# Kernel tuning notes

Measured on AMD Instinct MI355X. Metric: run time of the kernel, lower is better.

The kernel has to match this reference:

```python
import jax, jax.numpy as jnp
import numpy as np

DECAY = 0.999
EPS = 1e-05
COMMITMENT_COST = 0.25
M, D = 1024, 256
B, H, W = 32, 32, 32


def setup_inputs() -> dict:
    key = jax.random.key(0)
    k1, k2 = jax.random.split(key)
    init_bound = 1.0 / M
    x = jax.random.normal(k1, (B, H, W, D), dtype=jnp.float32)
    embedding = jax.random.uniform(k2, (M, D), dtype=jnp.float32,
                                   minval=-init_bound, maxval=init_bound)
    ema_count = jnp.zeros((M,), dtype=jnp.float32)
    ema_weight = embedding  # buffer initialized as embedding.clone()
    return {"x": x, "embedding": embedding, "ema_count": ema_count,
            "ema_weight": ema_weight}


def reference(x, embedding, ema_count, ema_weight):
    Mn, Dn = embedding.shape
    x_flat = jax.lax.stop_gradient(x).reshape(-1, Dn)          # [N, D]
    N = x_flat.shape[0]

    # (-cdist)^2 == squared euclidean distance; argmin is the same.
    x_sq = jnp.sum(x_flat * x_flat, axis=-1, keepdims=True)    # [N, 1]
    e_sq = jnp.sum(embedding * embedding, axis=-1)             # [M]
    distances = x_sq - 2.0 * (x_flat @ embedding.T) + e_sq[None, :]  # [N, M]
    indices = jnp.argmin(distances, axis=-1)                   # [N]

    quantized = embedding[indices].reshape(x.shape)            # gather

    # one-hot column sums == scatter-add of ones; encodings.T @ x_flat == scatter-add rows
    counts = jnp.zeros((Mn,), x.dtype).at[indices].add(1.0)    # [M]
    dw = jnp.zeros((Mn, Dn), x.dtype).at[indices].add(x_flat)  # [M, D]

    new_count = DECAY * ema_count + (1.0 - DECAY) * counts
    n = jnp.sum(new_count)
    new_count = (new_count + EPS) / (n + Mn * EPS) * n
    new_weight = DECAY * ema_weight + (1.0 - DECAY) * dw
    new_embedding = new_weight / new_count[:, None]

    codebook_loss = jnp.mean((jax.lax.stop_gradient(x) - quantized) ** 2)
    e_latent_loss = jnp.mean((x - jax.lax.stop_gradient(quantized)) ** 2)
    commitment_loss = COMMITMENT_COST * e_latent_loss

    quantized_st = x + jax.lax.stop_gradient(quantized - x)    # straight-through

    avg_probs = counts / N
    perplexity = jnp.exp(-jnp.sum(avg_probs * jnp.log(avg_probs + 1e-10)))

    return (quantized_st, commitment_loss, codebook_loss, perplexity,
            new_embedding, new_count, new_weight)
```

## Files before the change

kernel.cpp:

```cpp
#include <hip/hip_runtime.h>
#include <cfloat>
#include <math.h>

#define N_TOK 32768
#define DIM   256
#define MCODE 1024

typedef unsigned short u16;
typedef unsigned long long u64;
typedef __attribute__((ext_vector_type(8))) short short8;
typedef __attribute__((ext_vector_type(4))) float f32x4;

constexpr float DECAY_ = 0.999f;
constexpr float OMD_   = (float)(1.0 - 0.999);
constexpr float EPS_   = 1e-5f;
constexpr float MEPS_  = (float)(1024 * 1e-5);

constexpr int WS_EH   = 0;
constexpr int WS_EL   = 131072;
constexpr int WS_ESQ  = 262144;
constexpr int WS_CNTI = 263168;
constexpr int WS_BI   = 264192;
constexpr int WS_LP   = 296960;
constexpr int WS_KEY  = 299008;

constexpr int OUT_Q        = 0;
constexpr int OUT_COMMIT   = 8388608;
constexpr int OUT_CODEBOOK = 8388609;
constexpr int OUT_PERP     = 8388610;
constexpr int OUT_NE       = 8388611;
constexpr int OUT_NC       = 8650755;
constexpr int OUT_NW       = 8651779;

static __device__ __forceinline__ u16 f2bf(float f) {
    unsigned u = __float_as_uint(f);
    unsigned r = (u + 0x7fff + ((u >> 16) & 1)) >> 16;
    return (u16)r;
}
static __device__ __forceinline__ float bf2f(u16 h) {
    return __uint_as_float(((unsigned)h) << 16);
}
static __device__ __forceinline__ void gl2lds16(const u16* g, char* l) {
    __builtin_amdgcn_global_load_lds(
        (const __attribute__((address_space(1))) unsigned int*)g,
        (__attribute__((address_space(3))) unsigned int*)l, 16, 0, 0);
}
static __device__ __forceinline__ unsigned fmap(float f) {
    unsigned u = __float_as_uint(f);
    return (u & 0x80000000u) ? ~u : (u | 0x80000000u);
}

static __device__ __forceinline__ void load_row8(const float* __restrict__ src,
                                                 int wave_id, int lane,
                                                 float* vv, size_t* o) {
    int rb = wave_id >> 6, kc = (wave_id >> 3) & 7, t = wave_id & 7;
    int row = rb * 128 + t * 16 + (lane & 15);
    int k   = kc * 32 + (lane >> 4) * 8;
    const float* s = &src[row * DIM + k];
    float4 v0 = *(const float4*)s, v1 = *(const float4*)(s + 4);
    vv[0]=v0.x; vv[1]=v0.y; vv[2]=v0.z; vv[3]=v0.w;
    vv[4]=v1.x; vv[5]=v1.y; vv[6]=v1.z; vv[7]=v1.w;
    *o = (size_t)wave_id * 512 + lane * 8;
}
static __device__ __forceinline__ void pack_wave_hi(const float* __restrict__ src,
                                                    u16* __restrict__ dh,
                                                    int wave_id, int lane) {
    float vv[8]; size_t o;
    load_row8(src, wave_id, lane, vv, &o);
    short8 hv;
#pragma unroll
    for (int j = 0; j < 8; ++j) hv[j] = (short)f2bf(vv[j]);
    *(short8*)&dh[o] = hv;
}
static __device__ __forceinline__ void pack_wave_hl(const float* __restrict__ src,
                                                    u16* __restrict__ dh,
                                                    u16* __restrict__ dl,
                                                    int wave_id, int lane) {
    float vv[8]; size_t o;
    load_row8(src, wave_id, lane, vv, &o);
    short8 hv, lv;
#pragma unroll
    for (int j = 0; j < 8; ++j) {
        u16 h = f2bf(vv[j]);
        hv[j] = (short)h;
        lv[j] = (short)f2bf(vv[j] - bf2f(h));
    }
    *(short8*)&dh[o] = hv;
    *(short8*)&dl[o] = lv;
}

__global__ __launch_bounds__(256) void vq_setup(const float* __restrict__ x,
                                                const float* __restrict__ emb,
                                                u16* __restrict__ xh,
                                                u16* __restrict__ eh,
                                                u16* __restrict__ el,
                                                float* __restrict__ esq,
                                                u64* __restrict__ keys,
                                                int* __restrict__ cnti) {
    const int b = blockIdx.x, tid = threadIdx.x;
    const int lane = tid & 63, w = tid >> 6;
    if (b < 4096) { pack_wave_hi(x, xh, b * 4 + w, lane); return; }
    const int p = b - 4096;
    if (p < 128) {
        pack_wave_hl(emb, eh, el, p * 4 + w, lane);
    } else if (p < 384) {
        int c = (p - 128) * 4 + w;
        float4 v = *(const float4*)&emb[c * DIM + lane * 4];
        float s = v.x * v.x + v.y * v.y + v.z * v.z + v.w * v.w;
#pragma unroll
        for (int off = 32; off; off >>= 1) s += __shfl_xor(s, off, 64);
        if (lane == 0) esq[c] = s;
    } else if (p < 512) {
        keys[(p - 384) * 256 + tid] = ~0ULL;
    } else {
#pragma unroll
        for (int i = 0; i < 4; ++i) cnti[i * 256 + tid] = 0;
    }
}

__global__ __launch_bounds__(256) void vq_scores_mfma(const u16* __restrict__ xh,
                                                      const u16* __restrict__ eh,
                                                      const u16* __restrict__ el,
                                                      const float* __restrict__ esq,
                                                      u64* __restrict__ keys) {
    __shared__ __align__(16) char smem[33792];
    const int tid  = threadIdx.x;
    const int lane = tid & 63, w = tid >> 6;
    const int wm = w & 1, wn = w >> 1;
    const int raw = blockIdx.x;
    const int rb = (raw >> 6) * 8 + (raw & 7);
    const int cs = (raw >> 3) & 7;

    const u16* gb0 = xh + (size_t)rb * 32768;
    const u16* gb1 = eh + (size_t)cs * 32768;
    const u16* gb2 = el + (size_t)cs * 32768;

    const short8* Ah = (const short8*)(smem);
    const short8* Bh = (const short8*)(smem + 8192);
    const short8* Bl = (const short8*)(smem + 16384);

    f32x4 acc[4][4];
#pragma unroll
    for (int i = 0; i < 4; ++i)
#pragma unroll
        for (int j = 0; j < 4; ++j) acc[i][j] = (f32x4)0.f;

    for (int kc = 0; kc < 8; ++kc) {
        __syncthreads();
#pragma unroll
        for (int j = 0; j < 6; ++j) {
            int t = w * 6 + j;
            int arr = t >> 3, slot = t & 7;
            const u16* g = (arr == 0 ? gb0 : (arr == 1 ? gb1 : gb2))
                           + kc * 4096 + slot * 512 + lane * 8;
            gl2lds16(g, smem + arr * 8192 + slot * 1024);
        }
        __syncthreads();

        short8 ah[4];
#pragma unroll
        for (int tm = 0; tm < 4; ++tm)
            ah[tm] = Ah[(wm * 4 + tm) * 64 + lane];
#pragma unroll
        for (int tn = 0; tn < 4; ++tn) {
            int bidx = (wn * 4 + tn) * 64 + lane;
            short8 bh = Bh[bidx], bl = Bl[bidx];
#pragma unroll
            for (int tm = 0; tm < 4; ++tm) {
                acc[tm][tn] = __builtin_amdgcn_mfma_f32_16x16x32_bf16(ah[tm], bh, acc[tm][tn], 0, 0, 0);
                acc[tm][tn] = __builtin_amdgcn_mfma_f32_16x16x32_bf16(ah[tm], bl, acc[tm][tn], 0, 0, 0);
            }
        }
    }

    __syncthreads();
    float* cv = (float*)smem;
    int*   ci = (int*)(smem + 16896);
    const int ln = lane & 15, quad = lane >> 4;
#pragma unroll
    for (int tm = 0; tm < 4; ++tm) {
        float bv[4];
        int   bi[4];
#pragma unroll
        for (int r = 0; r < 4; ++r) { bv[r] = FLT_MAX; bi[r] = 0; }
#pragma unroll
        for (int tn = 0; tn < 4; ++tn) {
            int c = cs * 128 + wn * 64 + tn * 16 + ln;
            float ec = esq[c];
#pragma unroll
            for (int r = 0; r < 4; ++r) {
                float d = fmaf(-2.f, acc[tm][tn][r], ec);
                if (d < bv[r]) { bv[r] = d; bi[r] = c; }
            }
        }
        int row0 = wm * 64 + tm * 16 + quad * 4;
        int slot = wn * 16 + ln;
#pragma unroll
        for (int r = 0; r < 4; ++r) {
            cv[(row0 + r) * 33 + slot] = bv[r];
            ci[(row0 + r) * 33 + slot] = bi[r];
        }
    }
    __syncthreads();
    if (tid < 128) {
        float bv = cv[tid * 33];
        int   bi = ci[tid * 33];
#pragma unroll
        for (int s = 1; s < 32; ++s) {
            float v = cv[tid * 33 + s];
            int  ix = ci[tid * 33 + s];
            if (v < bv || (v == bv && ix < bi)) { bv = v; bi = ix; }
        }
        u64 key = ((u64)fmap(bv) << 32) | (unsigned)bi;
        atomicMin(&keys[rb * 128 + tid], key);
    }
}

__global__ __launch_bounds__(256) void vq_quant(const float* __restrict__ x,
                                                const float* __restrict__ emb,
                                                const u64* __restrict__ keys,
                                                float* __restrict__ outq,
                                                int* __restrict__ cnti,
                                                int* __restrict__ bi_arr,
                                                float* __restrict__ lpart) {
    const int tid = threadIdx.x, lane = tid & 63, w = tid >> 6;
    const float4* x4 = (const float4*)x;
    const float4* e4 = (const float4*)emb;
    float4* o4 = (float4*)outq;
    float lacc = 0.f;
#pragma unroll
    for (int it = 0; it < 4; ++it) {
        int row = blockIdx.x * 16 + it * 4 + w;
        int bi = (int)(unsigned)(keys[row] & 0xffffffffULL);
        if (lane == 0) { atomicAdd(&cnti[bi], 1); bi_arr[row] = bi; }
        float4 xv = x4[row * 64 + lane];
        float4 ev = e4[bi * 64 + lane];
        float4 q;
        q.x = xv.x + (ev.x - xv.x);  q.y = xv.y + (ev.y - xv.y);
        q.z = xv.z + (ev.z - xv.z);  q.w = xv.w + (ev.w - xv.w);
        o4[row * 64 + lane] = q;
        float dx = xv.x - ev.x, dy = xv.y - ev.y, dz = xv.z - ev.z, dwv = xv.w - ev.w;
        lacc += dx * dx + dy * dy + dz * dz + dwv * dwv;
    }
#pragma unroll
    for (int off = 32; off; off >>= 1) lacc += __shfl_xor(lacc, off, 64);
    __shared__ float red[4];
    if (lane == 0) red[w] = lacc;
    __syncthreads();
    if (tid == 0) lpart[blockIdx.x] = red[0] + red[1] + red[2] + red[3];
}

#define MEGA_CAP 6144
__global__ __launch_bounds__(256) void vq_mega(const float* __restrict__ x,
                                               const float* __restrict__ ema_count,
                                               const float* __restrict__ ema_weight,
                                               const int* __restrict__ cnti,
                                               const int* __restrict__ bi_arr,
                                               const float* __restrict__ lpart,
                                               float* __restrict__ out) {
    const int m = blockIdx.x, tid = threadIdx.x;
    __shared__ float fs[256];
    __shared__ int list[MEGA_CAP];
    __shared__ int lcount;

    float rsum = 0.f;
#pragma unroll
    for (int i = 0; i < 4; ++i) rsum += ema_count[tid * 4 + i];
    fs[tid] = rsum;
    if (tid == 0) lcount = 0;
    __syncthreads();
    for (int s = 128; s; s >>= 1) { if (tid < s) fs[tid] += fs[tid + s]; __syncthreads(); }
    const float n = DECAY_ * fs[0] + OMD_ * (float)N_TOK;
    __syncthreads();

    const int4* b4 = (const int4*)bi_arr;
#pragma unroll 4
    for (int i = tid; i < N_TOK / 4; i += 256) {
        int4 v = b4[i];
        if (v.x == m) { int p = atomicAdd(&lcount, 1); if (p < MEGA_CAP) list[p] = 4 * i; }
        if (v.y == m) { int p = atomicAdd(&lcount, 1); if (p < MEGA_CAP) list[p] = 4 * i + 1; }
        if (v.z == m) { int p = atomicAdd(&lcount, 1); if (p < MEGA_CAP) list[p] = 4 * i + 2; }
        if (v.w == m) { int p = atomicAdd(&lcount, 1); if (p < MEGA_CAP) list[p] = 4 * i + 3; }
    }
    __syncthreads();
    const int nm = lcount;
    float dwsum;
    if (nm <= MEGA_CAP) {
        float a0 = 0.f, a1 = 0.f, a2 = 0.f, a3 = 0.f;
        int i = 0;
        for (; i + 4 <= nm; i += 4) {
            a0 += x[list[i]     * DIM + tid];
            a1 += x[list[i + 1] * DIM + tid];
            a2 += x[list[i + 2] * DIM + tid];
            a3 += x[list[i + 3] * DIM + tid];
        }
        for (; i < nm; ++i) a0 += x[list[i] * DIM + tid];
        dwsum = (a0 + a1) + (a2 + a3);
    } else {
        __shared__ int chunk[256];
        float a0 = 0.f;
        for (int base = 0; base < N_TOK; base += 256) {
            __syncthreads();
            chunk[tid] = bi_arr[base + tid];
            __syncthreads();
            for (int j = 0; j < 256; ++j)
                if (chunk[j] == m) a0 += x[(base + j) * DIM + tid];
        }
        dwsum = a0;
    }

    float raw_m = DECAY_ * ema_count[m] + OMD_ * (float)nm;
    float ncm = (raw_m + EPS_) / (n + MEPS_) * n;
    float nw = DECAY_ * ema_weight[m * DIM + tid] + OMD_ * dwsum;
    out[OUT_NW + m * DIM + tid] = nw;
    out[OUT_NE + m * DIM + tid] = nw / ncm;
    if (tid == 0) out[OUT_NC + m] = ncm;

    if (m == 0) {
        float ent = 0.f;
#pragma unroll
        for (int i = 0; i < 4; ++i) {
            float p = (float)cnti[tid * 4 + i] / (float)N_TOK;
            ent += p * logf(p + 1e-10f);
        }
        __syncthreads();
        fs[tid] = ent;
        __syncthreads();
        for (int s = 128; s; s >>= 1) { if (tid < s) fs[tid] += fs[tid + s]; __syncthreads(); }
        float entr = fs[0];
        __syncthreads();
        float ls = 0.f;
#pragma unroll
        for (int k = 0; k < 8; ++k) ls += lpart[tid + 256 * k];
        fs[tid] = ls;
        __syncthreads();
        for (int s = 128; s; s >>= 1) { if (tid < s) fs[tid] += fs[tid + s]; __syncthreads(); }
        if (tid == 0) {
            float mean = fs[0] / (float)(N_TOK * DIM);
            out[OUT_COMMIT]   = 0.25f * mean;
            out[OUT_CODEBOOK] = mean;
            out[OUT_PERP]     = expf(-entr);
        }
    }
}

extern "C" void kernel_launch(void* const* d_in, const int* in_sizes, int n_in,
                              void* d_out, int out_size, void* d_ws, size_t ws_size,
                              hipStream_t stream) {
    const float* x          = (const float*)d_in[0];
    const float* emb        = (const float*)d_in[1];
    const float* ema_count  = (const float*)d_in[2];
    const float* ema_weight = (const float*)d_in[3];
    float* out = (float*)d_out;
    float* wf  = (float*)d_ws;

    u16* xh = (u16*)d_out;
    u16* eh = (u16*)(wf + WS_EH);
    u16* el = (u16*)(wf + WS_EL);

    float* esq    = wf + WS_ESQ;
    int*   cnti   = (int*)(wf + WS_CNTI);
    int*   bi_arr = (int*)(wf + WS_BI);
    float* lpart  = wf + WS_LP;
    u64*   keys   = (u64*)(wf + WS_KEY);

    vq_setup<<<4609, 256, 0, stream>>>(x, emb, xh, eh, el, esq, keys, cnti);
    vq_scores_mfma<<<2048, 256, 0, stream>>>(xh, eh, el, esq, keys);
    vq_quant<<<2048, 256, 0, stream>>>(x, emb, keys, out, cnti, bi_arr, lpart);
    vq_mega<<<MCODE, 256, 0, stream>>>(x, ema_count, ema_weight, cnti, bi_arr,
                                       lpart, out);
}
```

Before: 162.3 us.

## Double-buffer LDS staging in MFMA score kernel to overlap loads with compute

The score GEMM kernel now keeps two LDS buffers and prefetches the chunk two K-steps ahead with async global-to-LDS loads. Manual vmcnt waits and raw barriers replace the per-iteration pair of __syncthreads, and all fragments are read into registers before the barrier so the next stage can be issued into the same buffer. MFMA issue gets raised wave priority. This is meant to hide global load latency behind the MFMAs, at the cost of 48KB of LDS per block (lower occupancy) and fragile hand-written wait counts.

```diff
diff --git a/kernel.cpp b/kernel.cpp
--- a/kernel.cpp
+++ b/kernel.cpp
@@ -123,7 +123,7 @@
                                                       const u16* __restrict__ el,
                                                       const float* __restrict__ esq,
                                                       u64* __restrict__ keys) {
-    __shared__ __align__(16) char smem[33792];
+    __shared__ __align__(16) char smem[49152];
     const int tid  = threadIdx.x;
     const int lane = tid & 63, w = tid >> 6;
     const int wm = w & 1, wn = w >> 1;
@@ -135,43 +135,65 @@
     const u16* gb1 = eh + (size_t)cs * 32768;
     const u16* gb2 = el + (size_t)cs * 32768;
 
-    const short8* Ah = (const short8*)(smem);
-    const short8* Bh = (const short8*)(smem + 8192);
-    const short8* Bl = (const short8*)(smem + 16384);
-
-    f32x4 acc[4][4];
-#pragma unroll
-    for (int i = 0; i < 4; ++i)
-#pragma unroll
-        for (int j = 0; j < 4; ++j) acc[i][j] = (f32x4)0.f;
-
-    for (int kc = 0; kc < 8; ++kc) {
-        __syncthreads();
+    auto STAGE = [&](int KC, int BUF) {
 #pragma unroll
         for (int j = 0; j < 6; ++j) {
             int t = w * 6 + j;
             int arr = t >> 3, slot = t & 7;
             const u16* g = (arr == 0 ? gb0 : (arr == 1 ? gb1 : gb2))
-                           + kc * 4096 + slot * 512 + lane * 8;
-            gl2lds16(g, smem + arr * 8192 + slot * 1024);
-        }
-        __syncthreads();
-
-        short8 ah[4];
+                           + KC * 4096 + slot * 512 + lane * 8;
+            gl2lds16(g, smem + BUF * 24576 + arr * 8192 + slot * 1024);
+        }
+    };
+
+    f32x4 acc[4][4];
+#pragma unroll
+    for (int i = 0; i < 4; ++i)
+#pragma unroll
+        for (int j = 0; j < 4; ++j) acc[i][j] = (f32x4)0.f;
+
+    STAGE(0, 0);
+    STAGE(1, 1);
+    asm volatile("s_waitcnt vmcnt(6)" ::: "memory");
+    __builtin_amdgcn_s_barrier();
+
+#pragma unroll
+    for (int kc = 0; kc < 8; ++kc) {
+        const int buf = kc & 1;
+        const short8* Ah = (const short8*)(smem + buf * 24576);
+        const short8* Bh = (const short8*)(smem + buf * 24576 + 8192);
+        const short8* Bl = (const short8*)(smem + buf * 24576 + 16384);
+
+        short8 ah[4], bh[4], bl[4];
 #pragma unroll
         for (int tm = 0; tm < 4; ++tm)
             ah[tm] = Ah[(wm * 4 + tm) * 64 + lane];
 #pragma unroll
         for (int tn = 0; tn < 4; ++tn) {
-            int bidx = (wn * 4 + tn) * 64 + lane;
-            short8 bh = Bh[bidx], bl = Bl[bidx];
+            bh[tn] = Bh[(wn * 4 + tn) * 64 + lane];
+            bl[tn] = Bl[(wn * 4 + tn) * 64 + lane];
+        }
+        asm volatile("s_waitcnt lgkmcnt(0)" ::: "memory");
+        __builtin_amdgcn_sched_barrier(0);
+        __builtin_amdgcn_s_barrier();
+
+        if (kc < 6) STAGE(kc + 2, buf);
+
+        __builtin_amdgcn_s_setprio(1);
+#pragma unroll
+        for (int tn = 0; tn < 4; ++tn)
 #pragma unroll
             for (int tm = 0; tm < 4; ++tm) {
-                acc[tm][tn] = __builtin_amdgcn_mfma_f32_16x16x32_bf16(ah[tm], bh, acc[tm][tn], 0, 0, 0);
-                acc[tm][tn] = __builtin_amdgcn_mfma_f32_16x16x32_bf16(ah[tm], bl, acc[tm][tn], 0, 0, 0);
+                acc[tm][tn] = __builtin_amdgcn_mfma_f32_16x16x32_bf16(ah[tm], bh[tn], acc[tm][tn], 0, 0, 0);
+                acc[tm][tn] = __builtin_amdgcn_mfma_f32_16x16x32_bf16(ah[tm], bl[tn], acc[tm][tn], 0, 0, 0);
             }
-        }
-    }
+        __builtin_amdgcn_s_setprio(0);
+
+        if (kc < 6)       { asm volatile("s_waitcnt vmcnt(6)" ::: "memory"); }
+        else if (kc == 6) { asm volatile("s_waitcnt vmcnt(0)" ::: "memory"); }
+        if (kc < 7) __builtin_amdgcn_s_barrier();
+    }
+    __builtin_amdgcn_sched_barrier(0);
 
     __syncthreads();
     float* cv = (float*)smem;
```

New measurement: 218.4 us. 1.35x slower.
